# Optimization experiments

Measured on AMD Instinct MI355X. Metric: run time of the kernel, lower is better.

The kernel has to match this reference:

```python
import jax, jax.numpy as jnp
import numpy as np
import math

B, C, BINS, W = 2, 8, 1024, 512
HEADS = 16
HD = BINS // HEADS          # 64 head dim
ROT = BINS // HEADS // 2    # 32 rotated dims
EXP = 4
EPS = 1e-5
MAX_FREQ = 10.0


def setup_inputs() -> dict:
    key = jax.random.key(0)
    ks = jax.random.split(key, 8)
    def u(k, shape, fan_in):
        lim = 1.0 / math.sqrt(fan_in)
        return jax.random.uniform(k, shape, jnp.float32, -lim, lim)
    return {
        "x": jax.random.normal(ks[0], (B, C, BINS, W), jnp.float32),
        "norm1_w": jnp.ones((BINS,), jnp.float32),
        "norm1_b": jnp.zeros((BINS,), jnp.float32),
        # 'pixel' rotary init: linspace(1, max_freq/2, dim//2) * pi (learned)
        "rot_freqs": jnp.linspace(1.0, MAX_FREQ / 2, ROT // 2, dtype=jnp.float32) * math.pi,
        "q_w": u(ks[1], (C, BINS, BINS), BINS),
        "out_w": u(ks[2], (C, BINS, BINS), BINS),
        "norm2_w": jnp.ones((BINS,), jnp.float32),
        "norm2_b": jnp.zeros((BINS,), jnp.float32),
        "lin1_w": u(ks[3], (C, BINS * EXP, BINS), BINS),
        "lin2_w": u(ks[4], (C, BINS, BINS * EXP), BINS * EXP),
    }


def _mlin(x, w):
    # x: [b,c,f_in,w]; w: [c,f_out,f_in] -> [b,c,f_out,w]
    return jnp.einsum('bcfw,cgf->bcgw', x, w)


def _frame_norm(x, w, b):
    # LayerNorm over the bins axis (axis=2) of [b,c,bins,w]
    m = jnp.mean(x, axis=2, keepdims=True)
    v = jnp.var(x, axis=2, keepdims=True)
    xn = (x - m) * jax.lax.rsqrt(v + EPS)
    return xn * w[:, None] + b[:, None]


def _rotate(q, cos, sin):
    # q: [b,c,h,w,d]; rotate first ROT dims with interleaved-pair rotate_half
    q1, q2 = q[..., :ROT], q[..., ROT:]
    qp = q1.reshape(*q1.shape[:-1], ROT // 2, 2)
    rh = jnp.stack([-qp[..., 1], qp[..., 0]], axis=-1).reshape(q1.shape)
    return jnp.concatenate([q1 * cos + rh * sin, q2], axis=-1)


def _attention(x, rot_freqs, q_w, out_w):
    b, c, bins, w = x.shape
    # faithful to source: q, k, v ALL use q_proj
    y = _mlin(x, q_w)  # [b,c,bins,w]
    # -> [b,c,h,w,d]
    y = y.transpose(0, 1, 3, 2).reshape(b, c, w, HEADS, HD).transpose(0, 1, 3, 2, 4)
    # rotary angles: t * freqs, repeat-interleaved x2 -> [w, ROT]
    t = jnp.arange(w, dtype=jnp.float32)
    ang = jnp.repeat(t[:, None] * rot_freqs[None, :], 2, axis=-1)
    cos, sin = jnp.cos(ang), jnp.sin(ang)
    q = _rotate(y, cos, sin)
    k = _rotate(y, cos, sin)
    v = y
    # NOTE: source scales by 1/sqrt(h) where h == bins (spectral height)
    scores = jnp.einsum('bchwd,bchud->bchwu', q, k) / math.sqrt(bins)
    a = jnp.einsum('bchwu,bchud->bchwd', jax.nn.softmax(scores, axis=-1), v)
    # [b,c,h,w,d] -> [b,c,bins,w]
    a = a.transpose(0, 1, 3, 2, 4).reshape(b, c, w, bins).transpose(0, 1, 3, 2)
    return _mlin(a, out_w)


def reference(x, norm1_w, norm1_b, rot_freqs, q_w, out_w,
              norm2_w, norm2_b, lin1_w, lin2_w):
    z = _frame_norm(x, norm1_w, norm1_b)
    z = _attention(z, rot_freqs, q_w, out_w)
    x = x + z  # dropout=0 -> identity
    z = _frame_norm(x, norm2_w, norm2_b)
    z = _mlin(jax.nn.gelu(_mlin(z, lin1_w), approximate=False), lin2_w)
    return x + z
```

## Files before the change

### kernel.cpp

```cpp
#include <hip/hip_runtime.h>
#include <math.h>

#define BB 2
#define CCH 8
#define BINS 1024
#define WW 512
#define HEADS 16
#define HD 64
#define ROTD 32
#define EXPF 4
#define NXE 8388608L
#define NTW 32

typedef unsigned short ushortT;
typedef short bf16x8 __attribute__((ext_vector_type(8)));
typedef float f32x4 __attribute__((ext_vector_type(4)));

__device__ __forceinline__ ushortT f2bf(float f) {
    unsigned int u = __float_as_uint(f);
    u = (u + 0x7FFF + ((u >> 16) & 1)) >> 16;
    return (ushortT)u;
}
__device__ __forceinline__ float bf2f(ushortT h) {
    return __uint_as_float(((unsigned int)h) << 16);
}
__device__ __forceinline__ float geluf(float x) {
    return 0.5f * x * (1.f + erff(x * 0.70710678118654752f));
}
__device__ __forceinline__ void gl_lds16(const ushortT* g, ushortT* l) {
    __builtin_amdgcn_global_load_lds(
        (const __attribute__((address_space(1))) unsigned int*)g,
        (__attribute__((address_space(3))) unsigned int*)l, 16, 0, 0);
}

__global__ __launch_bounds__(1024)
void normT_k(const float* __restrict__ X, const float* __restrict__ wgt,
             const float* __restrict__ bia, ushortT* __restrict__ YT)
{
    __shared__ float tile[NTW][BINS + 1];
    __shared__ float red0[32][NTW], red1[32][NTW];
    __shared__ float ms[NTW], is[NTW];
    const int bc = blockIdx.x >> 4;
    const int w0 = (blockIdx.x & 15) * NTW;
    const int tid = threadIdx.x;
    const int w  = tid & (NTW - 1);
    const int fy = tid >> 5;
    const float* Xb = X + (long)bc * BINS * WW + w0;
    float s = 0.f, s2 = 0.f;
    for (int f = fy; f < BINS; f += 32) {
        float v = Xb[(long)f * WW + w];
        s += v; s2 += v * v;
        tile[w][f] = v;
    }
    red0[fy][w] = s; red1[fy][w] = s2;
    __syncthreads();
    if (tid < NTW) {
        float ss = 0.f, qq = 0.f;
        #pragma unroll
        for (int j = 0; j < 32; ++j) { ss += red0[j][tid]; qq += red1[j][tid]; }
        float m = ss * (1.f / BINS);
        float var = qq * (1.f / BINS) - m * m;
        ms[tid] = m; is[tid] = rsqrtf(var + 1e-5f);
    }
    __syncthreads();
    const int w2 = tid >> 5;
    const int c  = tid & 31;
    float m = ms[w2], inv = is[w2];
    ushortT* Yb = YT + ((long)bc * WW + w0 + w2) * BINS;
    #pragma unroll
    for (int jj = 0; jj < 4; ++jj) {
        int f0 = jj * 256 + c * 8;
        union { ushortT h[8]; uint4 v; } r;
        #pragma unroll
        for (int e = 0; e < 8; ++e) {
            int f = f0 + e;
            float v = (tile[w2][f] - m) * inv * wgt[f] + bia[f];
            r.h[e] = f2bf(v);
        }
        *(uint4*)&Yb[f0] = r.v;
    }
}

__global__ void rope_tab_k(const float* __restrict__ freqs,
                           float* __restrict__ cosT, float* __restrict__ sinT)
{
    int idx = blockIdx.x * 256 + threadIdx.x;
    if (idx >= WW * 16) return;
    int w = idx >> 4, i = idx & 15;
    float ang = (float)w * freqs[i];
    cosT[idx] = cosf(ang);
    sinT[idx] = sinf(ang);
}

__global__ __launch_bounds__(256)
void ropeB_k(const ushortT* __restrict__ yT, const float* __restrict__ cosT,
             const float* __restrict__ sinT, ushortT* __restrict__ rotT)
{
    long e0 = ((long)blockIdx.x * 256 + threadIdx.x) * 8;
    if (e0 >= NXE) return;
    int g0 = (int)(e0 & 1023);
    int w  = (int)((e0 >> 10) & 511);
    int d0 = g0 & 63;
    union { uint4 v; ushortT h8[8]; } in, ov;
    in.v = *(const uint4*)&yT[e0];
    if (d0 >= ROTD) {
        *(uint4*)&rotT[e0] = in.v;
        return;
    }
    #pragma unroll
    for (int j = 0; j < 8; j += 2) {
        int i = (d0 + j) >> 1;
        float c = cosT[w * 16 + i], s = sinT[w * 16 + i];
        float a = bf2f(in.h8[j]), b = bf2f(in.h8[j + 1]);
        ov.h8[j]     = f2bf(a * c - b * s);
        ov.h8[j + 1] = f2bf(b * c + a * s);
    }
    *(uint4*)&rotT[e0] = ov.v;
}

__global__ __launch_bounds__(256)
void mattn_k(const ushortT* __restrict__ rotT, const ushortT* __restrict__ yT,
             ushortT* __restrict__ oT)
{
    __shared__ ushortT Qs[64 * 64];
    __shared__ ushortT Ks[64 * 64];
    __shared__ ushortT Vs[64 * 72];
    __shared__ ushortT Ps[64 * 72];
    const int z = blockIdx.y;
    const int bc = z >> 4, h = z & 15;
    const int wq0 = blockIdx.x * 64;
    const int tid = threadIdx.x;
    const int wv = tid >> 6, l = tid & 63;
    const int lr = l & 15, lk = l >> 4;
    const long hbase = (long)bc * WW * 1024 + h * 64;

    #pragma unroll
    for (int p = 0; p < 2; ++p) {
        int r0 = p * 32 + wv * 8;
        int row = r0 + (l >> 3);
        int gs = (l & 7) ^ (row & 7);
        gl_lds16(rotT + hbase + (long)(wq0 + row) * 1024 + gs * 8, Qs + r0 * 64);
    }

    f32x4 oacc[4] = {};
    float mrow[4] = {-INFINITY, -INFINITY, -INFINITY, -INFINITY};
    float lrow[4] = {0.f, 0.f, 0.f, 0.f};

    for (int u0 = 0; u0 < WW; u0 += 64) {
        #pragma unroll
        for (int p = 0; p < 2; ++p) {
            int r0 = p * 32 + wv * 8;
            int row = r0 + (l >> 3);
            int gs = (l & 7) ^ (row & 7);
            gl_lds16(rotT + hbase + (long)(u0 + row) * 1024 + gs * 8, Ks + r0 * 64);
        }
        #pragma unroll
        for (int rep = 0; rep < 2; ++rep) {
            int ch = rep * 4 + wv;
            union { uint4 v; ushortT h8[8]; } tmp;
            tmp.v = *(const uint4*)(yT + hbase + (long)(u0 + l) * 1024 + ch * 8);
            #pragma unroll
            for (int j = 0; j < 8; ++j)
                Vs[(ch * 8 + j) * 72 + l] = tmp.h8[j];
        }
        __syncthreads();

        f32x4 sacc[4] = {};
        #pragma unroll
        for (int ko = 0; ko < 2; ++ko) {
            int ar = wv * 16 + lr;
            bf16x8 aq = *(const bf16x8*)&Qs[ar * 64 + (((ko * 4) + lk) ^ (ar & 7)) * 8];
            #pragma unroll
            for (int f = 0; f < 4; ++f) {
                int br = f * 16 + lr;
                bf16x8 bk = *(const bf16x8*)&Ks[br * 64 + (((ko * 4) + lk) ^ (br & 7)) * 8];
                sacc[f] = __builtin_amdgcn_mfma_f32_16x16x32_bf16(aq, bk, sacc[f], 0, 0, 0);
            }
        }

        #pragma unroll
        for (int rg = 0; rg < 4; ++rg) {
            float s0 = sacc[0][rg] * (1.f / 32.f);
            float s1 = sacc[1][rg] * (1.f / 32.f);
            float s2 = sacc[2][rg] * (1.f / 32.f);
            float s3 = sacc[3][rg] * (1.f / 32.f);
            float mx = fmaxf(fmaxf(s0, s1), fmaxf(s2, s3));
            mx = fmaxf(mx, __shfl_xor(mx, 1));
            mx = fmaxf(mx, __shfl_xor(mx, 2));
            mx = fmaxf(mx, __shfl_xor(mx, 4));
            mx = fmaxf(mx, __shfl_xor(mx, 8));
            float mnew = fmaxf(mrow[rg], mx);
            float al = __expf(mrow[rg] - mnew);
            float p0 = __expf(s0 - mnew), p1 = __expf(s1 - mnew);
            float p2 = __expf(s2 - mnew), p3 = __expf(s3 - mnew);
            float rs = p0 + p1 + p2 + p3;
            rs += __shfl_xor(rs, 1);
            rs += __shfl_xor(rs, 2);
            rs += __shfl_xor(rs, 4);
            rs += __shfl_xor(rs, 8);
            lrow[rg] = lrow[rg] * al + rs;
            mrow[rg] = mnew;
            oacc[0][rg] *= al; oacc[1][rg] *= al;
            oacc[2][rg] *= al; oacc[3][rg] *= al;
            int prow = wv * 16 + lk * 4 + rg;
            Ps[prow * 72 +  0 + lr] = f2bf(p0);
            Ps[prow * 72 + 16 + lr] = f2bf(p1);
            Ps[prow * 72 + 32 + lr] = f2bf(p2);
            Ps[prow * 72 + 48 + lr] = f2bf(p3);
        }
        asm volatile("s_waitcnt lgkmcnt(0)" ::: "memory");

        #pragma unroll
        for (int ko = 0; ko < 2; ++ko) {
            int ar = wv * 16 + lr;
            bf16x8 ap = *(const bf16x8*)&Ps[ar * 72 + ko * 32 + lk * 8];
            #pragma unroll
            for (int f = 0; f < 4; ++f) {
                bf16x8 bv = *(const bf16x8*)&Vs[(f * 16 + lr) * 72 + ko * 32 + lk * 8];
                oacc[f] = __builtin_amdgcn_mfma_f32_16x16x32_bf16(ap, bv, oacc[f], 0, 0, 0);
            }
        }
        __syncthreads();
    }

    #pragma unroll
    for (int rg = 0; rg < 4; ++rg) {
        float inv = 1.f / lrow[rg];
        int w = wq0 + wv * 16 + lk * 4 + rg;
        long b2 = (long)bc * WW * 1024 + (long)w * 1024 + h * 64;
        #pragma unroll
        for (int f = 0; f < 4; ++f)
            oT[b2 + f * 16 + lr] = f2bf(oacc[f][rg] * inv);
    }
}

template<bool HASRES, bool GELUF, bool TRANSOUT>
__global__ __launch_bounds__(256)
void fgemm_k(const float* __restrict__ A, long sA, int aMod,
             const ushortT* __restrict__ B, long sB,
             void* __restrict__ Cp, long sC,
             const float* __restrict__ R, long sR,
             int M, int N, int K, int gx, int gy)
{
    __shared__ ushortT smem[2 * 8192];
    ushortT* As = smem;
    ushortT* Bs = smem + 8192;
    const int nwg = gridDim.x;
    const int bid = blockIdx.x;
    const int lid = (bid & 7) * (nwg >> 3) + (bid >> 3);
    const int x = lid % gx;
    const int y = (lid / gx) % gy;
    const int z = lid / (gx * gy);
    const float*   Ab = A + (long)(z % aMod) * sA + (long)y * 128 * K;
    const ushortT* Bb = B + (long)z * sB + (long)x * 128 * K;
    const int tid = threadIdx.x;
    const int wv = tid >> 6, l = tid & 63;
    const int lrow = l & 15, lk = l >> 4;
    const int mb = (wv >> 1) * 64, nb = (wv & 1) * 64;
    const int arow = tid >> 3, agrp = tid & 7;
    f32x4 acc[4][4] = {};
    float4 a0[4], a1[4];
    const int NT = K >> 6;

    auto fetchA = [&](int k0) {
        #pragma unroll
        for (int c = 0; c < 4; ++c) {
            const float* src = Ab + (long)(arow + c * 32) * K + k0 + agrp * 8;
            a0[c] = *(const float4*)src;
            a1[c] = *(const float4*)(src + 4);
        }
    };
    auto commitA = [&]() {
        #pragma unroll
        for (int c = 0; c < 4; ++c) {
            int row = arow + c * 32;
            union { ushortT h[8]; uint4 v; } r;
            r.h[0] = f2bf(a0[c].x); r.h[1] = f2bf(a0[c].y);
            r.h[2] = f2bf(a0[c].z); r.h[3] = f2bf(a0[c].w);
            r.h[4] = f2bf(a1[c].x); r.h[5] = f2bf(a1[c].y);
            r.h[6] = f2bf(a1[c].z); r.h[7] = f2bf(a1[c].w);
            *(uint4*)&As[row * 64 + ((agrp ^ (row & 7)) << 3)] = r.v;
        }
    };
    auto stageB = [&](int k0) {
        #pragma unroll
        for (int t = 0; t < 4; ++t) {
            int r0 = wv * 32 + t * 8;
            int row = r0 + (l >> 3);
            int gs = (l & 7) ^ (row & 7);
            gl_lds16(Bb + (long)row * K + k0 + gs * 8, Bs + r0 * 64);
        }
    };
    auto compute = [&]() {
        #pragma unroll
        for (int ko = 0; ko < 2; ++ko) {
            bf16x8 af[4], bg[4];
            #pragma unroll
            for (int i = 0; i < 4; ++i) {
                int ra = mb + i * 16 + lrow;
                af[i] = *(const bf16x8*)&As[ra * 64 + ((lk + ko * 4) ^ (ra & 7)) * 8];
                int rb = nb + i * 16 + lrow;
                bg[i] = *(const bf16x8*)&Bs[rb * 64 + ((lk + ko * 4) ^ (rb & 7)) * 8];
            }
            #pragma unroll
            for (int i = 0; i < 4; ++i)
                #pragma unroll
                for (int j = 0; j < 4; ++j)
                    acc[i][j] = __builtin_amdgcn_mfma_f32_16x16x32_bf16(
                        af[i], bg[j], acc[i][j], 0, 0, 0);
        }
    };

    fetchA(0);
    for (int t = 0; t < NT; ++t) {
        __builtin_amdgcn_s_barrier();
        __builtin_amdgcn_sched_barrier(0);
        stageB(t << 6);
        __builtin_amdgcn_sched_barrier(0);
        commitA();
        if (t + 1 < NT) {
            fetchA((t + 1) << 6);
            __builtin_amdgcn_sched_barrier(0);
            asm volatile("s_waitcnt vmcnt(8) lgkmcnt(0)" ::: "memory");
        } else {
            __builtin_amdgcn_sched_barrier(0);
            asm volatile("s_waitcnt vmcnt(0) lgkmcnt(0)" ::: "memory");
        }
        __builtin_amdgcn_s_barrier();
        __builtin_amdgcn_sched_barrier(0);
        compute();
    }

    const int m0g = y * 128 + mb, n0g = x * 128 + nb;
    if (!TRANSOUT) {
        float* Cf = (float*)Cp + (long)z * sC;
        #pragma unroll
        for (int i = 0; i < 4; ++i)
            #pragma unroll
            for (int j = 0; j < 4; ++j)
                #pragma unroll
                for (int rg = 0; rg < 4; ++rg) {
                    long m = m0g + i * 16 + lk * 4 + rg;
                    long n = n0g + j * 16 + lrow;
                    float v = acc[i][j][rg];
                    if (GELUF) v = geluf(v);
                    if (HASRES) v += R[(long)z * sR + m * N + n];
                    Cf[m * N + n] = v;
                }
    } else {
        ushortT* Ts = smem + wv * 4096;
        __syncthreads();
        #pragma unroll
        for (int i = 0; i < 4; ++i)
            #pragma unroll
            for (int j = 0; j < 4; ++j)
                #pragma unroll
                for (int rg = 0; rg < 4; ++rg) {
                    int ml = i * 16 + lk * 4 + rg;
                    int nl = j * 16 + lrow;
                    float v = acc[i][j][rg];
                    if (GELUF) v = geluf(v);
                    Ts[nl * 64 + (((ml >> 3) ^ (nl & 7)) << 3) + (ml & 7)] = f2bf(v);
                }
        __syncthreads();
        ushortT* CT = (ushortT*)Cp + (long)z * sC;
        #pragma unroll
        for (int p = 0; p < 8; ++p) {
            int nl = p * 8 + (l >> 3), mc = l & 7;
            uint4 d = *(const uint4*)&Ts[nl * 64 + ((mc ^ (nl & 7)) << 3)];
            *(uint4*)&CT[(long)(n0g + nl) * M + m0g + mc * 8] = d;
        }
    }
}

extern "C" void kernel_launch(void* const* d_in, const int* in_sizes, int n_in,
                              void* d_out, int out_size, void* d_ws, size_t ws_size,
                              hipStream_t stream)
{
    const float* x    = (const float*)d_in[0];
    const float* n1w  = (const float*)d_in[1];
    const float* n1b  = (const float*)d_in[2];
    const float* freqs= (const float*)d_in[3];
    const float* qw   = (const float*)d_in[4];
    const float* ow   = (const float*)d_in[5];
    const float* n2w  = (const float*)d_in[6];
    const float* n2b  = (const float*)d_in[7];
    const float* l1w  = (const float*)d_in[8];
    const float* l2w  = (const float*)d_in[9];
    float* out = (float*)d_out;
    char* wsb  = (char*)d_ws;
    const long MB = 1L << 20;

    ushortT* znT  = (ushortT*)(wsb +   0 * MB);
    ushortT* yT   = (ushortT*)(wsb +  16 * MB);
    ushortT* rotT = (ushortT*)(wsb +  32 * MB);
    ushortT* CfT  = (ushortT*)(wsb +  48 * MB);
    ushortT* zn2T = (ushortT*)(wsb +  64 * MB);
    ushortT* h1T  = (ushortT*)(wsb +  80 * MB);
    float*   cosT = (float*)  (wsb + 144 * MB);
    float*   sinT = cosT + WW * 16;

    rope_tab_k<<<32, 256, 0, stream>>>(freqs, cosT, sinT);

    normT_k<<<BB * CCH * 16, 1024, 0, stream>>>(x, n1w, n1b, znT);

    fgemm_k<false, false, true><<<512, 256, 0, stream>>>(
        qw,  (long)BINS * BINS, CCH,
        znT, (long)WW * BINS,
        yT,  (long)WW * BINS,
        nullptr, 0, BINS, WW, BINS, 4, 8);

    ropeB_k<<<4096, 256, 0, stream>>>(yT, cosT, sinT, rotT);

    mattn_k<<<dim3(8, 256), 256, 0, stream>>>(rotT, yT, CfT);

    fgemm_k<true, false, false><<<512, 256, 0, stream>>>(
        ow,  (long)BINS * BINS, CCH,
        CfT, (long)WW * BINS,
        out, (long)BINS * WW,
        x,   (long)BINS * WW, BINS, WW, BINS, 4, 8);

    normT_k<<<BB * CCH * 16, 1024, 0, stream>>>(out, n2w, n2b, zn2T);

    fgemm_k<false, true, true><<<2048, 256, 0, stream>>>(
        l1w,  (long)BINS * EXPF * BINS, CCH,
        zn2T, (long)WW * BINS,
        h1T,  (long)WW * BINS * EXPF,
        nullptr, 0, BINS * EXPF, WW, BINS, 4, 32);

    fgemm_k<true, false, false><<<512, 256, 0, stream>>>(
        l2w, (long)BINS * BINS * EXPF, CCH,
        h1T, (long)WW * BINS * EXPF,
        out, (long)BINS * WW,
        out, (long)BINS * WW, BINS, WW, BINS * EXPF, 4, 8);
}
```

Measured before the change: 436.4 us.

## Double-buffer B tiles in fgemm and pack bf16 conversion with v_cvt_pk

```diff
diff --git a/kernel.cpp b/kernel.cpp
--- a/kernel.cpp
+++ b/kernel.cpp
@@ -23,6 +23,11 @@
 }
 __device__ __forceinline__ float bf2f(ushortT h) {
     return __uint_as_float(((unsigned int)h) << 16);
+}
+__device__ __forceinline__ unsigned int cvtpk(float lo, float hi) {
+    unsigned int r;
+    asm("v_cvt_pk_bf16_f32 %0, %1, %2" : "=v"(r) : "v"(lo), "v"(hi));
+    return r;
 }
 __device__ __forceinline__ float geluf(float x) {
     return 0.5f * x * (1.f + erff(x * 0.70710678118654752f));
@@ -242,9 +247,8 @@
              const float* __restrict__ R, long sR,
              int M, int N, int K, int gx, int gy)
 {
-    __shared__ ushortT smem[2 * 8192];
+    __shared__ ushortT smem[3 * 8192];
     ushortT* As = smem;
-    ushortT* Bs = smem + 8192;
     const int nwg = gridDim.x;
     const int bid = blockIdx.x;
     const int lid = (bid & 7) * (nwg >> 3) + (bid >> 3);
@@ -274,24 +278,26 @@
         #pragma unroll
         for (int c = 0; c < 4; ++c) {
             int row = arow + c * 32;
-            union { ushortT h[8]; uint4 v; } r;
-            r.h[0] = f2bf(a0[c].x); r.h[1] = f2bf(a0[c].y);
-            r.h[2] = f2bf(a0[c].z); r.h[3] = f2bf(a0[c].w);
-            r.h[4] = f2bf(a1[c].x); r.h[5] = f2bf(a1[c].y);
-            r.h[6] = f2bf(a1[c].z); r.h[7] = f2bf(a1[c].w);
-            *(uint4*)&As[row * 64 + ((agrp ^ (row & 7)) << 3)] = r.v;
+            uint4 v;
+            v.x = cvtpk(a0[c].x, a0[c].y);
+            v.y = cvtpk(a0[c].z, a0[c].w);
+            v.z = cvtpk(a1[c].x, a1[c].y);
+            v.w = cvtpk(a1[c].z, a1[c].w);
+            *(uint4*)&As[row * 64 + ((agrp ^ (row & 7)) << 3)] = v;
         }
     };
-    auto stageB = [&](int k0) {
+    auto stageB = [&](int k0, int buf) {
+        ushortT* BsB = smem + 8192 + buf * 8192;
         #pragma unroll
         for (int t = 0; t < 4; ++t) {
             int r0 = wv * 32 + t * 8;
             int row = r0 + (l >> 3);
             int gs = (l & 7) ^ (row & 7);
-            gl_lds16(Bb + (long)row * K + k0 + gs * 8, Bs + r0 * 64);
+            gl_lds16(Bb + (long)row * K + k0 + gs * 8, BsB + r0 * 64);
         }
     };
-    auto compute = [&]() {
+    auto compute = [&](int buf) {
+        const ushortT* BsB = smem + 8192 + buf * 8192;
         #pragma unroll
         for (int ko = 0; ko < 2; ++ko) {
             bf16x8 af[4], bg[4];
@@ -300,7 +306,7 @@
                 int ra = mb + i * 16 + lrow;
                 af[i] = *(const bf16x8*)&As[ra * 64 + ((lk + ko * 4) ^ (ra & 7)) * 8];
                 int rb = nb + i * 16 + lrow;
-                bg[i] = *(const bf16x8*)&Bs[rb * 64 + ((lk + ko * 4) ^ (rb & 7)) * 8];
+                bg[i] = *(const bf16x8*)&BsB[rb * 64 + ((lk + ko * 4) ^ (rb & 7)) * 8];
             }
             #pragma unroll
             for (int i = 0; i < 4; ++i)
@@ -312,23 +318,31 @@
     };
 
     fetchA(0);
+    stageB(0, 0);
+    commitA();
+    if (NT > 1) {
+        fetchA(64);
+        stageB(64, 1);
+        asm volatile("s_waitcnt vmcnt(12) lgkmcnt(0)" ::: "memory");
+    } else {
+        asm volatile("s_waitcnt vmcnt(0) lgkmcnt(0)" ::: "memory");
+    }
+    __builtin_amdgcn_s_barrier();
+
     for (int t = 0; t < NT; ++t) {
+        compute(t & 1);
         __builtin_amdgcn_s_barrier();
-        __builtin_amdgcn_sched_barrier(0);
-        stageB(t << 6);
-        __builtin_amdgcn_sched_barrier(0);
-        commitA();
         if (t + 1 < NT) {
-            fetchA((t + 1) << 6);
-            __builtin_amdgcn_sched_barrier(0);
-            asm volatile("s_waitcnt vmcnt(8) lgkmcnt(0)" ::: "memory");
-        } else {
-            __builtin_amdgcn_sched_barrier(0);
-            asm volatile("s_waitcnt vmcnt(0) lgkmcnt(0)" ::: "memory");
-        }
-        __builtin_amdgcn_s_barrier();
-        __builtin_amdgcn_sched_barrier(0);
-        compute();
+            commitA();
+            if (t + 2 < NT) {
+                fetchA((t + 2) << 6);
+                stageB((t + 2) << 6, t & 1);
+                asm volatile("s_waitcnt vmcnt(12) lgkmcnt(0)" ::: "memory");
+            } else {
+                asm volatile("s_waitcnt vmcnt(0) lgkmcnt(0)" ::: "memory");
+            }
+            __builtin_amdgcn_s_barrier();
+        }
     }
 
     const int m0g = y * 128 + mb, n0g = x * 128 + nb;
```

Result: no change. 434.7 us (-0.4%).
